# Kernel tuning notes

Measured on AMD Instinct MI355X. Metric: run time of the kernel, lower is better.

## Reference

```python
import math
import jax, jax.numpy as jnp
import numpy as np

L, H, D, V = 12, 12, 768, 50257
DH = D // H
B, TV, TT = 4, 64, 448
EPS = 1e-5


def setup_inputs() -> dict:
    key = jax.random.key(0)
    ks = jax.random.split(key, 10)
    w = lambda i, shape: jax.random.normal(ks[i], shape, jnp.float32) * 0.02
    return {
        "x": jax.random.randint(ks[0], (B, TT), 0, V, dtype=jnp.int32),
        "visual_embeds": jax.random.normal(ks[1], (B, TV, D), jnp.float32),
        "wte": w(2, (V, D)),
        "wpe": w(3, (1024, D)),
        "ln1_w": jnp.ones((L, D), jnp.float32),
        "ln1_b": jnp.zeros((L, D), jnp.float32),
        "attn_w": w(4, (L, D, 3 * D)),
        "attn_b": jnp.zeros((L, 3 * D), jnp.float32),
        "proj_w": w(5, (L, D, D)),
        "proj_b": jnp.zeros((L, D), jnp.float32),
        "ln2_w": jnp.ones((L, D), jnp.float32),
        "ln2_b": jnp.zeros((L, D), jnp.float32),
        "fc_w": w(6, (L, D, 4 * D)),
        "fc_b": jnp.zeros((L, 4 * D), jnp.float32),
        "fc2_w": w(7, (L, 4 * D, D)),
        "fc2_b": jnp.zeros((L, D), jnp.float32),
        "lnf_w": jnp.ones((D,), jnp.float32),
        "lnf_b": jnp.zeros((D,), jnp.float32),
    }


def layernorm(x, w, b):
    mu = jnp.mean(x, axis=-1, keepdims=True)
    var = jnp.mean(jnp.square(x - mu), axis=-1, keepdims=True)
    return (x - mu) * jax.lax.rsqrt(var + EPS) * w + b


def gpt_forward(x, visual_embeds, wte, wpe, ln1_w, ln1_b, attn_w, attn_b,
                proj_w, proj_b, ln2_w, ln2_b, fc_w, fc_b, fc2_w, fc2_b,
                lnf_w, lnf_b):
    text = wte[x]                                          # [B,TT,D]
    h = jnp.concatenate([visual_embeds, text], axis=1)     # [B,T,D]
    T = h.shape[1]
    h = h + wpe[:T][None]                                  # position embeddings
    # Faithful to source: the boolean causal mask is ADDED to the scores
    # (att = att + mask), i.e. +1.0 on allowed positions, +0.0 elsewhere.
    mask = jnp.tril(jnp.ones((T, T), jnp.float32))[None, None]  # [1,1,T,T]
    scale = 1.0 / math.sqrt(DH)

    def block(h, p):
        l1w, l1b, aw, ab, pw, pb, l2w, l2b, fw, fb, f2w, f2b = p
        n = layernorm(h, l1w, l1b)
        qkv = n @ aw + ab                                  # [B,T,3D]
        q, k, v = jnp.split(qkv, 3, axis=-1)
        q = q.reshape(B, T, H, DH).transpose(0, 2, 1, 3)   # [B,H,T,DH]
        k = k.reshape(B, T, H, DH).transpose(0, 2, 1, 3)
        v = v.reshape(B, T, H, DH).transpose(0, 2, 1, 3)
        att = jnp.einsum('bhqd,bhkd->bhqk', q, k) * scale + mask
        att = jax.nn.softmax(att, axis=-1)
        o = jnp.einsum('bhqk,bhkd->bhqd', att, v)
        o = o.transpose(0, 2, 1, 3).reshape(B, T, D)
        h = h + (o @ pw + pb)
        n = layernorm(h, l2w, l2b)
        m = jax.nn.gelu(n @ fw + fb, approximate=False) @ f2w + f2b
        return h + m, None

    params = (ln1_w, ln1_b, attn_w, attn_b, proj_w, proj_b,
              ln2_w, ln2_b, fc_w, fc_b, fc2_w, fc2_b)
    h, _ = jax.lax.scan(block, h, params)
    h = layernorm(h, lnf_w, lnf_b)
    logits = h @ wte.T                                     # tied embedding head
    return logits


def reference(x, visual_embeds, wte, wpe, ln1_w, ln1_b, attn_w, attn_b,
              proj_w, proj_b, ln2_w, ln2_b, fc_w, fc_b, fc2_w, fc2_b,
              lnf_w, lnf_b):
    return gpt_forward(x, visual_embeds, wte, wpe, ln1_w, ln1_b, attn_w,
                       attn_b, proj_w, proj_b, ln2_w, ln2_b, fc_w, fc_b,
                       fc2_w, fc2_b, lnf_w, lnf_b)
```

## Files before the change

### kernel.cpp

```cpp
#include <hip/hip_runtime.h>
#include <math.h>
#include <stdint.h>

constexpr int L  = 12;
constexpr int H  = 12;
constexpr int D  = 768;
constexpr int V  = 50257;
constexpr int DH = 64;
constexpr int B  = 4;
constexpr int TV = 64;
constexpr int TT = 448;
constexpr int T  = TV + TT;
constexpr int M  = B * T;

using bf16x8 = __attribute__((ext_vector_type(8))) __bf16;
using f32x4  = __attribute__((ext_vector_type(4))) float;

__device__ __forceinline__ ushort bfhi(float x) { return (ushort)(__float_as_uint(x) >> 16); }
__device__ __forceinline__ float  bfup(ushort h) { return __uint_as_float(((unsigned)h) << 16); }

__device__ __forceinline__ float gelu_exact(float v) {
    return 0.5f * v * (1.0f + erff(v * 0.7071067811865476f));
}

__device__ __forceinline__ void gload16(const void* g, void* l) {
    __builtin_amdgcn_global_load_lds(
        (const __attribute__((address_space(1))) unsigned int*)(uintptr_t)g,
        (__attribute__((address_space(3))) unsigned int*)(uintptr_t)l,
        16, 0, 0);
}

__global__ __launch_bounds__(256) void embed_kernel(
    const int* __restrict__ x, const float* __restrict__ vis,
    const float* __restrict__ wte, const float* __restrict__ wpe,
    float* __restrict__ h)
{
    const int row = blockIdx.x;
    const int b = row / T, t = row % T;
    const float* src;
    if (t < TV) src = vis + ((size_t)b * TV + t) * D;
    else        src = wte + (size_t)x[b * TT + (t - TV)] * D;
    const float* pe = wpe + (size_t)t * D;
    float* dst = h + (size_t)row * D;
    for (int i = threadIdx.x; i < D; i += blockDim.x)
        dst[i] = src[i] + pe[i];
}

__global__ __launch_bounds__(256) void ln_kernel(
    const float* __restrict__ in, const float* __restrict__ w,
    const float* __restrict__ bb, ushort* __restrict__ ohi,
    ushort* __restrict__ olo)
{
    const int row = blockIdx.x;
    const float* xr = in + (size_t)row * D;
    float s = 0.f, s2 = 0.f;
    for (int i = threadIdx.x; i < D; i += blockDim.x) {
        float v = xr[i];
        s += v; s2 += v * v;
    }
    #pragma unroll
    for (int off = 32; off; off >>= 1) {
        s  += __shfl_down(s,  off);
        s2 += __shfl_down(s2, off);
    }
    __shared__ float ls[4], ls2[4];
    const int wid = threadIdx.x >> 6, lane = threadIdx.x & 63;
    if (lane == 0) { ls[wid] = s; ls2[wid] = s2; }
    __syncthreads();
    if (threadIdx.x == 0) {
        float a = 0.f, c = 0.f;
        for (int i = 0; i < 4; ++i) { a += ls[i]; c += ls2[i]; }
        ls[0] = a; ls2[0] = c;
    }
    __syncthreads();
    const float mean = ls[0] / D;
    const float var  = ls2[0] / D - mean * mean;
    const float inv  = rsqrtf(var + 1e-5f);
    ushort* oh = ohi + (size_t)row * D;
    ushort* ol = olo + (size_t)row * D;
    for (int i = threadIdx.x; i < D; i += blockDim.x) {
        const float y = (xr[i] - mean) * inv * w[i] + bb[i];
        const ushort hh = bfhi(y);
        oh[i] = hh;
        ol[i] = bfhi(y - bfup(hh));
    }
}

__global__ __launch_bounds__(256) void wconv_t(
    const float* __restrict__ W, ushort* __restrict__ Phi,
    ushort* __restrict__ Plo, int K, int N)
{
    __shared__ float tbuf[32][33];
    const int n0 = blockIdx.x * 32, k0 = blockIdx.y * 32;
    const int tx = threadIdx.x & 31, ty = threadIdx.x >> 5;
    for (int r = ty; r < 32; r += 8)
        tbuf[r][tx] = W[(size_t)(k0 + r) * N + n0 + tx];
    __syncthreads();
    for (int r = ty; r < 32; r += 8) {
        const float v = tbuf[tx][r];
        const ushort hh = bfhi(v);
        const size_t idx = (size_t)(n0 + r) * K + k0 + tx;
        Phi[idx] = hh;
        Plo[idx] = bfhi(v - bfup(hh));
    }
}

template<int OUTM, bool DOGELU, bool DORES, bool BCONV>
__global__ __launch_bounds__(256, 2) void gemm_mfma(
    const ushort* __restrict__ Ahi, const ushort* __restrict__ Alo,
    const ushort* __restrict__ Bhi, const ushort* __restrict__ Blo,
    const float* __restrict__ Bf32, const float* __restrict__ bias,
    const float* res, float* Cf, ushort* Chi, ushort* Clo,
    int N, int K)
{
    __shared__ ushort lds[4][128][64];
    const int tid  = threadIdx.x;
    const int wave = tid >> 6, lane = tid & 63;
    const int rl = lane & 15, g = lane >> 4;
    const int wm = wave >> 1, wn = wave & 1;
    const int bm = blockIdx.y * 128;
    const int bn = blockIdx.x * 128;

    const int srow  = wave * 32 + (lane >> 3);
    const int sslot = (lane & 7) ^ (lane >> 3);
    const int brow = tid >> 1, bhalf = tid & 1;
    const int gnB  = bn + brow;

    f32x4 acc[4][4] = {};

    for (int k0 = 0; k0 < K; k0 += 64) {
        #pragma unroll
        for (int j = 0; j < 4; ++j) {
            const size_t gro = (size_t)(bm + srow + j * 8) * K + k0 + sslot * 8;
            gload16(Ahi + gro, &lds[0][0][0] + (wave * 4 + j) * 512);
            gload16(Alo + gro, &lds[1][0][0] + (wave * 4 + j) * 512);
        }
        if constexpr (!BCONV) {
            #pragma unroll
            for (int j = 0; j < 4; ++j) {
                const size_t gro = (size_t)(bn + srow + j * 8) * K + k0 + sslot * 8;
                gload16(Bhi + gro, &lds[2][0][0] + (wave * 4 + j) * 512);
                gload16(Blo + gro, &lds[3][0][0] + (wave * 4 + j) * 512);
            }
        } else {
            const bool bok = gnB < N;
            const float* bsrc = Bf32 + (size_t)gnB * K + k0 + bhalf * 32;
            #pragma unroll
            for (int i = 0; i < 8; ++i) {
                float4 v = bok ? *reinterpret_cast<const float4*>(bsrc + i * 4)
                               : make_float4(0.f, 0.f, 0.f, 0.f);
                ushort4 hv, lv;
                hv.x = bfhi(v.x); lv.x = bfhi(v.x - bfup(hv.x));
                hv.y = bfhi(v.y); lv.y = bfhi(v.y - bfup(hv.y));
                hv.z = bfhi(v.z); lv.z = bfhi(v.z - bfup(hv.z));
                hv.w = bfhi(v.w); lv.w = bfhi(v.w - bfup(hv.w));
                const int slot = bhalf * 4 + (i >> 1);
                const int doff = brow * 64 + ((slot ^ (brow & 7)) << 3) + (i & 1) * 4;
                *reinterpret_cast<ushort4*>(&lds[2][0][0] + doff) = hv;
                *reinterpret_cast<ushort4*>(&lds[3][0][0] + doff) = lv;
            }
        }
        __syncthreads();

        #pragma unroll
        for (int c = 0; c < 2; ++c) {
            bf16x8 aH[4], aL[4], bH[4], bL[4];
            const int sx = ((((c << 2) + g) ^ (rl & 7)) << 3);
            #pragma unroll
            for (int f = 0; f < 4; ++f) {
                const int mr = wm * 64 + f * 16 + rl;
                const int nr = wn * 64 + f * 16 + rl;
                aH[f] = *reinterpret_cast<const bf16x8*>(&lds[0][mr][0] + sx);
                aL[f] = *reinterpret_cast<const bf16x8*>(&lds[1][mr][0] + sx);
                bH[f] = *reinterpret_cast<const bf16x8*>(&lds[2][nr][0] + sx);
                bL[f] = *reinterpret_cast<const bf16x8*>(&lds[3][nr][0] + sx);
            }
            #pragma unroll
            for (int i = 0; i < 4; ++i)
                #pragma unroll
                for (int j = 0; j < 4; ++j) {
                    acc[i][j] = __builtin_amdgcn_mfma_f32_16x16x32_bf16(aH[i], bH[j], acc[i][j], 0, 0, 0);
                    acc[i][j] = __builtin_amdgcn_mfma_f32_16x16x32_bf16(aH[i], bL[j], acc[i][j], 0, 0, 0);
                    acc[i][j] = __builtin_amdgcn_mfma_f32_16x16x32_bf16(aL[i], bH[j], acc[i][j], 0, 0, 0);
                }
        }
        __syncthreads();
    }

    #pragma unroll
    for (int j = 0; j < 4; ++j) {
        const int ncol = bn + wn * 64 + j * 16 + rl;
        if (BCONV && ncol >= N) continue;
        const float bj = bias ? bias[ncol] : 0.f;
        #pragma unroll
        for (int i = 0; i < 4; ++i) {
            const int mrow = bm + wm * 64 + i * 16 + g * 4;
            #pragma unroll
            for (int r = 0; r < 4; ++r) {
                float v = acc[i][j][r] + bj;
                if (DOGELU) v = gelu_exact(v);
                const size_t idx = (size_t)(mrow + r) * N + ncol;
                if (DORES) v += res[idx];
                if (OUTM == 0) {
                    Cf[idx] = v;
                } else {
                    const ushort hh = bfhi(v);
                    Chi[idx] = hh;
                    Clo[idx] = bfhi(v - bfup(hh));
                }
            }
        }
    }
}

__global__ __launch_bounds__(256) void attn_scores_kernel(
    const float* __restrict__ qkv, float* __restrict__ att)
{
    const int bh = blockIdx.z;
    const int b = bh / H, hh = bh % H;
    const int bq = blockIdx.y * 64;
    const int bk = blockIdx.x * 64;
    const float* Q  = qkv + (size_t)b * T * 3 * D + hh * DH;
    const float* Kp = Q + D;

    __shared__ float Qs[16][65];
    __shared__ float Ks[16][65];
    const int tid = threadIdx.x;
    const int tx = tid & 15, ty = tid >> 4;
    const int r  = tid >> 2;
    const int d4 = (tid & 3) << 2;

    float acc[4][4] = {};

    for (int k0 = 0; k0 < DH; k0 += 16) {
        {
            float4 v = *reinterpret_cast<const float4*>(&Q[(size_t)(bq + r) * 3 * D + k0 + d4]);
            Qs[d4 + 0][r] = v.x; Qs[d4 + 1][r] = v.y;
            Qs[d4 + 2][r] = v.z; Qs[d4 + 3][r] = v.w;
        }
        {
            float4 v = *reinterpret_cast<const float4*>(&Kp[(size_t)(bk + r) * 3 * D + k0 + d4]);
            Ks[d4 + 0][r] = v.x; Ks[d4 + 1][r] = v.y;
            Ks[d4 + 2][r] = v.z; Ks[d4 + 3][r] = v.w;
        }
        __syncthreads();
        #pragma unroll
        for (int kk = 0; kk < 16; ++kk) {
            float a[4], b2[4];
            #pragma unroll
            for (int i = 0; i < 4; ++i) a[i]  = Qs[kk][ty * 4 + i];
            #pragma unroll
            for (int j = 0; j < 4; ++j) b2[j] = Ks[kk][tx * 4 + j];
            #pragma unroll
            for (int i = 0; i < 4; ++i)
                #pragma unroll
                for (int j = 0; j < 4; ++j)
                    acc[i][j] = fmaf(a[i], b2[j], acc[i][j]);
        }
        __syncthreads();
    }

    #pragma unroll
    for (int i = 0; i < 4; ++i) {
        const int q = bq + ty * 4 + i;
        #pragma unroll
        for (int j = 0; j < 4; ++j) {
            const int k = bk + tx * 4 + j;
            att[((size_t)bh * T + q) * T + k] =
                acc[i][j] * 0.125f + (k <= q ? 1.0f : 0.0f);
        }
    }
}

__global__ __launch_bounds__(64) void softmax_kernel(float* __restrict__ att)
{
    float* row = att + (size_t)blockIdx.x * T;
    const int lane = threadIdx.x;
    float v[8];
    float mx = -1e30f;
    #pragma unroll
    for (int i = 0; i < 8; ++i) { v[i] = row[lane + i * 64]; mx = fmaxf(mx, v[i]); }
    #pragma unroll
    for (int off = 32; off; off >>= 1) mx = fmaxf(mx, __shfl_xor(mx, off));
    float s = 0.f;
    #pragma unroll
    for (int i = 0; i < 8; ++i) { v[i] = __expf(v[i] - mx); s += v[i]; }
    #pragma unroll
    for (int off = 32; off; off >>= 1) s += __shfl_xor(s, off);
    const float inv = 1.0f / s;
    #pragma unroll
    for (int i = 0; i < 8; ++i) row[lane + i * 64] = v[i] * inv;
}

__global__ __launch_bounds__(256) void attn_pv_kernel(
    const float* __restrict__ att, const float* __restrict__ qkv,
    ushort* __restrict__ o_hi, ushort* __restrict__ o_lo)
{
    const int bh = blockIdx.z;
    const int b = bh / H, hh = bh % H;
    const int bq = blockIdx.y * 64;
    const float* Vp = qkv + (size_t)b * T * 3 * D + 2 * D + hh * DH;
    const float* Am = att + (size_t)bh * T * T;

    __shared__ float As[16][65];
    __shared__ float Vs[16][65];
    const int tid = threadIdx.x;
    const int tx = tid & 15, ty = tid >> 4;
    const int r  = tid >> 2;
    const int k4 = (tid & 3) << 2;

    float acc[4][4] = {};

    for (int k0 = 0; k0 < T; k0 += 16) {
        {
            float4 v = *reinterpret_cast<const float4*>(&Am[(size_t)(bq + r) * T + k0 + k4]);
            As[k4 + 0][r] = v.x; As[k4 + 1][r] = v.y;
            As[k4 + 2][r] = v.z; As[k4 + 3][r] = v.w;
        }
        {
            const int kk = tid >> 4;
            const int dd = (tid & 15) << 2;
            float4 v = *reinterpret_cast<const float4*>(&Vp[(size_t)(k0 + kk) * 3 * D + dd]);
            Vs[kk][dd + 0] = v.x; Vs[kk][dd + 1] = v.y;
            Vs[kk][dd + 2] = v.z; Vs[kk][dd + 3] = v.w;
        }
        __syncthreads();
        #pragma unroll
        for (int kk = 0; kk < 16; ++kk) {
            float a[4], b2[4];
            #pragma unroll
            for (int i = 0; i < 4; ++i) a[i]  = As[kk][ty * 4 + i];
            #pragma unroll
            for (int j = 0; j < 4; ++j) b2[j] = Vs[kk][tx * 4 + j];
            #pragma unroll
            for (int i = 0; i < 4; ++i)
                #pragma unroll
                for (int j = 0; j < 4; ++j)
                    acc[i][j] = fmaf(a[i], b2[j], acc[i][j]);
        }
        __syncthreads();
    }

    #pragma unroll
    for (int i = 0; i < 4; ++i) {
        const int q = bq + ty * 4 + i;
        #pragma unroll
        for (int j = 0; j < 4; ++j) {
            const int d = tx * 4 + j;
            const size_t idx = ((size_t)b * T + q) * D + hh * DH + d;
            const float v = acc[i][j];
            const ushort uh = bfhi(v);
            o_hi[idx] = uh;
            o_lo[idx] = bfhi(v - bfup(uh));
        }
    }
}

extern "C" void kernel_launch(void* const* d_in, const int* in_sizes, int n_in,
                              void* d_out, int out_size, void* d_ws, size_t ws_size,
                              hipStream_t stream)
{
    const int*   x      = (const int*)  d_in[0];
    const float* vis    = (const float*)d_in[1];
    const float* wte    = (const float*)d_in[2];
    const float* wpe    = (const float*)d_in[3];
    const float* ln1_w  = (const float*)d_in[4];
    const float* ln1_b  = (const float*)d_in[5];
    const float* attn_w = (const float*)d_in[6];
    const float* attn_b = (const float*)d_in[7];
    const float* proj_w = (const float*)d_in[8];
    const float* proj_b = (const float*)d_in[9];
    const float* ln2_w  = (const float*)d_in[10];
    const float* ln2_b  = (const float*)d_in[11];
    const float* fc_w   = (const float*)d_in[12];
    const float* fc_b   = (const float*)d_in[13];
    const float* fc2_w  = (const float*)d_in[14];
    const float* fc2_b  = (const float*)d_in[15];
    const float* lnf_w  = (const float*)d_in[16];
    const float* lnf_b  = (const float*)d_in[17];

    float* out = (float*)d_out;

    float*  h    = (float*)d_ws;
    ushort* n_hi = (ushort*)(h + (size_t)M * D);
    ushort* n_lo = n_hi + (size_t)M * D;

    float* qkv = out;
    float* att = qkv + (size_t)M * 3 * D;
    ushort* o_hi   = (ushort*)(att + (size_t)B * H * T * T);
    ushort* o_lo   = o_hi   + (size_t)M * D;
    ushort* mid_hi = o_lo   + (size_t)M * D;
    ushort* mid_lo = mid_hi + (size_t)M * 4 * D;
    ushort* wq_hi  = mid_lo + (size_t)M * 4 * D;
    ushort* wq_lo  = wq_hi  + (size_t)D * 3 * D;
    ushort* wp_hi  = wq_lo  + (size_t)D * 3 * D;
    ushort* wp_lo  = wp_hi  + (size_t)D * D;
    ushort* wf_hi  = wp_lo  + (size_t)D * D;
    ushort* wf_lo  = wf_hi  + (size_t)D * 4 * D;
    ushort* wf2_hi = wf_lo  + (size_t)D * 4 * D;
    ushort* wf2_lo = wf2_hi + (size_t)4 * D * D;

    embed_kernel<<<M, 256, 0, stream>>>(x, vis, wte, wpe, h);

    for (int l = 0; l < L; ++l) {
        ln_kernel<<<M, 256, 0, stream>>>(h, ln1_w + (size_t)l * D, ln1_b + (size_t)l * D,
                                         n_hi, n_lo);

        wconv_t<<<dim3(3 * D / 32, D / 32), 256, 0, stream>>>(
            attn_w + (size_t)l * D * 3 * D, wq_hi, wq_lo, D, 3 * D);
        gemm_mfma<0, false, false, false><<<dim3(3 * D / 128, M / 128), 256, 0, stream>>>(
            n_hi, n_lo, wq_hi, wq_lo, nullptr, attn_b + (size_t)l * 3 * D,
            nullptr, qkv, nullptr, nullptr, 3 * D, D);

        attn_scores_kernel<<<dim3(T / 64, T / 64, B * H), 256, 0, stream>>>(qkv, att);
        softmax_kernel<<<B * H * T, 64, 0, stream>>>(att);
        attn_pv_kernel<<<dim3(1, T / 64, B * H), 256, 0, stream>>>(att, qkv, o_hi, o_lo);

        wconv_t<<<dim3(D / 32, D / 32), 256, 0, stream>>>(
            proj_w + (size_t)l * D * D, wp_hi, wp_lo, D, D);
        gemm_mfma<0, false, true, false><<<dim3(D / 128, M / 128), 256, 0, stream>>>(
            o_hi, o_lo, wp_hi, wp_lo, nullptr, proj_b + (size_t)l * D,
            h, h, nullptr, nullptr, D, D);

        ln_kernel<<<M, 256, 0, stream>>>(h, ln2_w + (size_t)l * D, ln2_b + (size_t)l * D,
                                         n_hi, n_lo);

        wconv_t<<<dim3(4 * D / 32, D / 32), 256, 0, stream>>>(
            fc_w + (size_t)l * D * 4 * D, wf_hi, wf_lo, D, 4 * D);
        gemm_mfma<1, true, false, false><<<dim3(4 * D / 128, M / 128), 256, 0, stream>>>(
            n_hi, n_lo, wf_hi, wf_lo, nullptr, fc_b + (size_t)l * 4 * D,
            nullptr, nullptr, mid_hi, mid_lo, 4 * D, D);

        wconv_t<<<dim3(D / 32, 4 * D / 32), 256, 0, stream>>>(
            fc2_w + (size_t)l * 4 * D * D, wf2_hi, wf2_lo, 4 * D, D);
        gemm_mfma<0, false, true, false><<<dim3(D / 128, M / 128), 256, 0, stream>>>(
            mid_hi, mid_lo, wf2_hi, wf2_lo, nullptr, fc2_b + (size_t)l * D,
            h, h, nullptr, nullptr, D, 4 * D);
    }

    ln_kernel<<<M, 256, 0, stream>>>(h, lnf_w, lnf_b, n_hi, n_lo);

    gemm_mfma<0, false, false, true><<<dim3((V + 127) / 128, M / 128), 256, 0, stream>>>(
        n_hi, n_lo, nullptr, nullptr, wte, nullptr,
        nullptr, out, nullptr, nullptr, V, D);
}
```

Baseline: 5.590 ms.

## Halve GEMM K-tile for higher occupancy, add XCD-aware block remap

After: 6.092 ms. 9.0% more time.

```diff
diff --git a/kernel.cpp b/kernel.cpp
--- a/kernel.cpp
+++ b/kernel.cpp
@@ -106,47 +106,50 @@
 }
 
 template<int OUTM, bool DOGELU, bool DORES, bool BCONV>
-__global__ __launch_bounds__(256, 2) void gemm_mfma(
+__global__ __launch_bounds__(256, 4) void gemm_mfma(
     const ushort* __restrict__ Ahi, const ushort* __restrict__ Alo,
     const ushort* __restrict__ Bhi, const ushort* __restrict__ Blo,
     const float* __restrict__ Bf32, const float* __restrict__ bias,
     const float* res, float* Cf, ushort* Chi, ushort* Clo,
     int N, int K)
 {
-    __shared__ ushort lds[4][128][64];
+    __shared__ ushort lds[4][128][32];
     const int tid  = threadIdx.x;
     const int wave = tid >> 6, lane = tid & 63;
     const int rl = lane & 15, g = lane >> 4;
     const int wm = wave >> 1, wn = wave & 1;
-    const int bm = blockIdx.y * 128;
-    const int bn = blockIdx.x * 128;
-
-    const int srow  = wave * 32 + (lane >> 3);
-    const int sslot = (lane & 7) ^ (lane >> 3);
+
+    const unsigned q8  = gridDim.x >> 3;
+    const unsigned lin = (blockIdx.x & 7) * q8 + (blockIdx.x >> 3);
+    const int bm = (int)(lin & 15) * 128;
+    const int bn = (int)(lin >> 4) * 128;
+
+    const int srow  = lane >> 2;
+    const int sslot = (lane & 3) ^ ((lane >> 2) & 3);
     const int brow = tid >> 1, bhalf = tid & 1;
     const int gnB  = bn + brow;
 
     f32x4 acc[4][4] = {};
 
-    for (int k0 = 0; k0 < K; k0 += 64) {
-        #pragma unroll
-        for (int j = 0; j < 4; ++j) {
-            const size_t gro = (size_t)(bm + srow + j * 8) * K + k0 + sslot * 8;
-            gload16(Ahi + gro, &lds[0][0][0] + (wave * 4 + j) * 512);
-            gload16(Alo + gro, &lds[1][0][0] + (wave * 4 + j) * 512);
-        }
-        if constexpr (!BCONV) {
-            #pragma unroll
-            for (int j = 0; j < 4; ++j) {
-                const size_t gro = (size_t)(bn + srow + j * 8) * K + k0 + sslot * 8;
-                gload16(Bhi + gro, &lds[2][0][0] + (wave * 4 + j) * 512);
-                gload16(Blo + gro, &lds[3][0][0] + (wave * 4 + j) * 512);
+    for (int k0 = 0; k0 < K; k0 += 32) {
+        #pragma unroll
+        for (int j = 0; j < 2; ++j) {
+            const int cb = wave * 2 + j;
+            const int r  = cb * 16 + srow;
+            const size_t groA = (size_t)(bm + r) * K + k0 + sslot * 8;
+            gload16(Ahi + groA, &lds[0][0][0] + cb * 512);
+            gload16(Alo + groA, &lds[1][0][0] + cb * 512);
+            if constexpr (!BCONV) {
+                const size_t groB = (size_t)(bn + r) * K + k0 + sslot * 8;
+                gload16(Bhi + groB, &lds[2][0][0] + cb * 512);
+                gload16(Blo + groB, &lds[3][0][0] + cb * 512);
             }
-        } else {
+        }
+        if constexpr (BCONV) {
             const bool bok = gnB < N;
-            const float* bsrc = Bf32 + (size_t)gnB * K + k0 + bhalf * 32;
-            #pragma unroll
-            for (int i = 0; i < 8; ++i) {
+            const float* bsrc = Bf32 + (size_t)gnB * K + k0 + bhalf * 16;
+            #pragma unroll
+            for (int i = 0; i < 4; ++i) {
                 float4 v = bok ? *reinterpret_cast<const float4*>(bsrc + i * 4)
                                : make_float4(0.f, 0.f, 0.f, 0.f);
                 ushort4 hv, lv;
@@ -154,36 +157,34 @@
                 hv.y = bfhi(v.y); lv.y = bfhi(v.y - bfup(hv.y));
                 hv.z = bfhi(v.z); lv.z = bfhi(v.z - bfup(hv.z));
                 hv.w = bfhi(v.w); lv.w = bfhi(v.w - bfup(hv.w));
-                const int slot = bhalf * 4 + (i >> 1);
-                const int doff = brow * 64 + ((slot ^ (brow & 7)) << 3) + (i & 1) * 4;
+                const int sl   = bhalf * 2 + (i >> 1);
+                const int doff = brow * 32 + ((sl ^ (brow & 3)) << 3) + (i & 1) * 4;
                 *reinterpret_cast<ushort4*>(&lds[2][0][0] + doff) = hv;
                 *reinterpret_cast<ushort4*>(&lds[3][0][0] + doff) = lv;
             }
         }
         __syncthreads();
 
-        #pragma unroll
-        for (int c = 0; c < 2; ++c) {
-            bf16x8 aH[4], aL[4], bH[4], bL[4];
-            const int sx = ((((c << 2) + g) ^ (rl & 7)) << 3);
-            #pragma unroll
-            for (int f = 0; f < 4; ++f) {
-                const int mr = wm * 64 + f * 16 + rl;
-                const int nr = wn * 64 + f * 16 + rl;
-                aH[f] = *reinterpret_cast<const bf16x8*>(&lds[0][mr][0] + sx);
-                aL[f] = *reinterpret_cast<const bf16x8*>(&lds[1][mr][0] + sx);
-                bH[f] = *reinterpret_cast<const bf16x8*>(&lds[2][nr][0] + sx);
-                bL[f] = *reinterpret_cast<const bf16x8*>(&lds[3][nr][0] + sx);
+        bf16x8 aH[4], aL[4], bH[4], bL[4];
+        #pragma unroll
+        for (int f = 0; f < 4; ++f) {
+            const int mr = wm * 64 + f * 16 + rl;
+            const int nr = wn * 64 + f * 16 + rl;
+            const int sa = (g ^ (mr & 3)) << 3;
+            const int sb = (g ^ (nr & 3)) << 3;
+            aH[f] = *reinterpret_cast<const bf16x8*>(&lds[0][mr][0] + sa);
+            aL[f] = *reinterpret_cast<const bf16x8*>(&lds[1][mr][0] + sa);
+            bH[f] = *reinterpret_cast<const bf16x8*>(&lds[2][nr][0] + sb);
+            bL[f] = *reinterpret_cast<const bf16x8*>(&lds[3][nr][0] + sb);
+        }
+        #pragma unroll
+        for (int i = 0; i < 4; ++i)
+            #pragma unroll
+            for (int j = 0; j < 4; ++j) {
+                acc[i][j] = __builtin_amdgcn_mfma_f32_16x16x32_bf16(aH[i], bH[j], acc[i][j], 0, 0, 0);
+                acc[i][j] = __builtin_amdgcn_mfma_f32_16x16x32_bf16(aH[i], bL[j], acc[i][j], 0, 0, 0);
+                acc[i][j] = __builtin_amdgcn_mfma_f32_16x16x32_bf16(aL[i], bH[j], acc[i][j], 0, 0, 0);
             }
-            #pragma unroll
-            for (int i = 0; i < 4; ++i)
-                #pragma unroll
-                for (int j = 0; j < 4; ++j) {
-                    acc[i][j] = __builtin_amdgcn_mfma_f32_16x16x32_bf16(aH[i], bH[j], acc[i][j], 0, 0, 0);
-                    acc[i][j] = __builtin_amdgcn_mfma_f32_16x16x32_bf16(aH[i], bL[j], acc[i][j], 0, 0, 0);
-                    acc[i][j] = __builtin_amdgcn_mfma_f32_16x16x32_bf16(aL[i], bH[j], acc[i][j], 0, 0, 0);
-                }
-        }
         __syncthreads();
     }
 
@@ -202,7 +203,8 @@
                 const size_t idx = (size_t)(mrow + r) * N + ncol;
                 if (DORES) v += res[idx];
                 if (OUTM == 0) {
-                    Cf[idx] = v;
+                    if (BCONV) __builtin_nontemporal_store(v, &Cf[idx]);
+                    else       Cf[idx] = v;
                 } else {
                     const ushort hh = bfhi(v);
                     Chi[idx] = hh;
@@ -394,7 +396,8 @@
     ushort* wq_hi  = mid_lo + (size_t)M * 4 * D;
     ushort* wq_lo  = wq_hi  + (size_t)D * 3 * D;
     ushort* wp_hi  = wq_lo  + (size_t)D * 3 * D;
-    ushort* wp_lo  = wp_hi  + (size_t)D * D;
+    ushort* wp_hi_end = wp_hi + (size_t)D * D;
+    ushort* wp_lo  = wp_hi_end;
     ushort* wf_hi  = wp_lo  + (size_t)D * D;
     ushort* wf_lo  = wf_hi  + (size_t)D * 4 * D;
     ushort* wf2_hi = wf_lo  + (size_t)D * 4 * D;
@@ -408,7 +411,7 @@
 
         wconv_t<<<dim3(3 * D / 32, D / 32), 256, 0, stream>>>(
             attn_w + (size_t)l * D * 3 * D, wq_hi, wq_lo, D, 3 * D);
-        gemm_mfma<0, false, false, false><<<dim3(3 * D / 128, M / 128), 256, 0, stream>>>(
+        gemm_mfma<0, false, false, false><<<(3 * D / 128) * (M / 128), 256, 0, stream>>>(
             n_hi, n_lo, wq_hi, wq_lo, nullptr, attn_b + (size_t)l * 3 * D,
             nullptr, qkv, nullptr, nullptr, 3 * D, D);
 
@@ -418,7 +421,7 @@
 
         wconv_t<<<dim3(D / 32, D / 32), 256, 0, stream>>>(
             proj_w + (size_t)l * D * D, wp_hi, wp_lo, D, D);
-        gemm_mfma<0, false, true, false><<<dim3(D / 128, M / 128), 256, 0, stream>>>(
+        gemm_mfma<0, false, true, false><<<(D / 128) * (M / 128), 256, 0, stream>>>(
             o_hi, o_lo, wp_hi, wp_lo, nullptr, proj_b + (size_t)l * D,
             h, h, nullptr, nullptr, D, D);
 
@@ -427,20 +430,20 @@
 
         wconv_t<<<dim3(4 * D / 32, D / 32), 256, 0, stream>>>(
             fc_w + (size_t)l * D * 4 * D, wf_hi, wf_lo, D, 4 * D);
-        gemm_mfma<1, true, false, false><<<dim3(4 * D / 128, M / 128), 256, 0, stream>>>(
+        gemm_mfma<1, true, false, false><<<(4 * D / 128) * (M / 128), 256, 0, stream>>>(
             n_hi, n_lo, wf_hi, wf_lo, nullptr, fc_b + (size_t)l * 4 * D,
             nullptr, nullptr, mid_hi, mid_lo, 4 * D, D);
 
         wconv_t<<<dim3(D / 32, 4 * D / 32), 256, 0, stream>>>(
             fc2_w + (size_t)l * 4 * D * D, wf2_hi, wf2_lo, 4 * D, D);
-        gemm_mfma<0, false, true, false><<<dim3(D / 128, M / 128), 256, 0, stream>>>(
+        gemm_mfma<0, false, true, false><<<(D / 128) * (M / 128), 256, 0, stream>>>(
             mid_hi, mid_lo, wf2_hi, wf2_lo, nullptr, fc2_b + (size_t)l * D,
             h, h, nullptr, nullptr, D, 4 * D);
     }
 
     ln_kernel<<<M, 256, 0, stream>>>(h, lnf_w, lnf_b, n_hi, n_lo);
 
-    gemm_mfma<0, false, false, true><<<dim3((V + 127) / 128, M / 128), 256, 0, stream>>>(
+    gemm_mfma<0, false, false, true><<<((V + 127) / 128) * (M / 128), 256, 0, stream>>>(
         n_hi, n_lo, nullptr, nullptr, wte, nullptr,
         nullptr, out, nullptr, nullptr, V, D);
 }
```
